# Optimization experiments

Measured on AMD Instinct MI355X. Metric: run time of the kernel, lower is better.

Reference implementation:

```python
import jax, jax.numpy as jnp
import numpy as np

DIM = 128
N = 8192
E = 262144
EPS = 1e-8  # torch.cosine_similarity eps


def setup_inputs() -> dict:
    key = jax.random.key(0)
    k1, k2, k3, k4 = jax.random.split(key, 4)
    x = jax.random.normal(k1, (N, DIM), dtype=jnp.float32)
    edge_index = jax.random.randint(k2, (2, E), 0, N, dtype=jnp.int32)
    # GCNConv parameters: linear weight (glorot-ish) and bias
    W_gcn = jax.random.normal(k3, (DIM, DIM), dtype=jnp.float32) / np.sqrt(DIM)
    b_gcn = jnp.zeros((DIM,), dtype=jnp.float32)
    return {"x": x, "edge_index": edge_index, "W_gcn": W_gcn, "b_gcn": b_gcn}


def _cosine_attention(x):
    # torch.cosine_similarity(x.unsqueeze(1), x.unsqueeze(0), dim=-1)
    # == (x @ x.T) / max(||x_i|| * ||x_j||, eps)
    nrm = jnp.sqrt(jnp.sum(x * x, axis=-1))                      # [N]
    denom = jnp.maximum(nrm[:, None] * nrm[None, :], EPS)        # [N, N]
    sim = (x @ x.T) / denom                                      # [N, N]
    return jax.nn.sigmoid(sim @ x)                               # [N, dim]


def _gcn_conv(x, edge_index, W, b):
    n = x.shape[0]
    xw = x @ W                                                   # [N, dim]
    # add self-loops
    loops = jnp.arange(n, dtype=edge_index.dtype)
    row = jnp.concatenate([edge_index[0], loops])                # source
    col = jnp.concatenate([edge_index[1], loops])                # target
    # symmetric normalization: deg computed on target nodes
    deg = jax.ops.segment_sum(jnp.ones_like(col, dtype=x.dtype), col, num_segments=n)
    dis = jnp.where(deg > 0, jax.lax.rsqrt(jnp.maximum(deg, 1.0)), 0.0)
    dis = jnp.where(deg > 0, deg ** -0.5, 0.0)
    norm = dis[row] * dis[col]                                   # [E+N]
    msgs = xw[row] * norm[:, None]                               # [E+N, dim]
    out = jax.ops.segment_sum(msgs, col, num_segments=n)         # [N, dim]
    return out + b


def reference(x, edge_index, W_gcn, b_gcn):
    att = _cosine_attention(x)
    g = _gcn_conv(x, edge_index, W_gcn, b_gcn)
    return g * att
```

## Files before the change

kernel.cpp:

```cpp
#include <hip/hip_runtime.h>
#include <math.h>

#define NN   8192
#define DIM  128
#define NE   262144
#define XU   64
#define JCH  128
#define HBH  64
#define HEB  (NE / HBH)
#define GU   128
#define GR   64
#define SD   96
#define MSCALE 1048576.0f
#define MINV  (1.0f / 1048576.0f)

typedef __attribute__((ext_vector_type(8))) short bf16x8;
typedef __attribute__((ext_vector_type(4))) float f32x4;

static __device__ __forceinline__ unsigned short f2bf(float f) {
  unsigned int u = __float_as_uint(f);
  return (unsigned short)((u + 0x7FFFu + ((u >> 16) & 1u)) >> 16);
}
static __device__ __forceinline__ float bf2f(unsigned int h) {
  return __uint_as_float(h << 16);
}
static __device__ __forceinline__ unsigned int pk2(float a, float b) {
  return (unsigned int)f2bf(a) | ((unsigned int)f2bf(b) << 16);
}


static __device__ void ph_xtx(int u, int tid, char* smem,
    const float* __restrict__ x, float* __restrict__ rinv,
    int* __restrict__ Mi) {
  char* XTs = smem;
  char* XTu = smem + 32768;
  int j0 = u * JCH;
  int jl = tid >> 1, half = tid & 1;
  const float4* xr = (const float4*)(x + (size_t)(j0 + jl) * DIM + half * 64);
  float ss = 0.f;
  #pragma unroll
  for (int i = 0; i < 16; ++i) {
    float4 v = xr[i];
    ss += v.x * v.x + v.y * v.y + v.z * v.z + v.w * v.w;
  }
  ss += __shfl_xor(ss, 1);
  float rv = 1.0f / sqrtf(ss);
  if (half == 0) rinv[j0 + jl] = rv;
  #pragma unroll
  for (int c4 = 0; c4 < 16; ++c4) {
    float4 v = xr[c4];
    #pragma unroll
    for (int i = 0; i < 4; ++i) {
      int d = half * 64 + c4 * 4 + i;
      float f = ((const float*)&v)[i];
      int off = d * 256 + ((jl * 2) ^ ((d & 7) << 4));
      *(unsigned short*)(XTs + off) = f2bf(f * rv);
      *(unsigned short*)(XTu + off) = f2bf(f);
    }
  }
  __syncthreads();

  int w = tid >> 6, lane = tid & 63;
  int l15 = lane & 15, g16 = (lane >> 4) * 16, swz = (lane & 7) << 4;
  f32x4 acc[2][8];
  #pragma unroll
  for (int dt = 0; dt < 2; ++dt)
    #pragma unroll
    for (int ct = 0; ct < 8; ++ct) acc[dt][ct] = (f32x4){0.f, 0.f, 0.f, 0.f};
  #pragma unroll
  for (int ks = 0; ks < 4; ++ks) {
    int ko = (ks * 64 + g16) ^ swz;
    bf16x8 a0 = *(const bf16x8*)(XTs + (w * 32 + l15) * 256 + ko);
    bf16x8 a1 = *(const bf16x8*)(XTs + (w * 32 + 16 + l15) * 256 + ko);
    #pragma unroll
    for (int ct = 0; ct < 8; ++ct) {
      bf16x8 b = *(const bf16x8*)(XTu + (ct * 16 + l15) * 256 + ko);
      acc[0][ct] = __builtin_amdgcn_mfma_f32_16x16x32_bf16(a0, b, acc[0][ct], 0, 0, 0);
      acc[1][ct] = __builtin_amdgcn_mfma_f32_16x16x32_bf16(a1, b, acc[1][ct], 0, 0, 0);
    }
  }
  #pragma unroll
  for (int dt = 0; dt < 2; ++dt)
    #pragma unroll
    for (int ct = 0; ct < 8; ++ct)
      #pragma unroll
      for (int r = 0; r < 4; ++r) {
        int row = w * 32 + dt * 16 + (lane >> 4) * 4 + r;
        int col = ct * 16 + l15;
        atomicAdd(&Mi[row * DIM + col],
                  __float2int_rn(acc[dt][ct][r] * MSCALE));
      }
}

static __device__ void ph_histplace(int h, int tid, int* ldeg,
    const int* __restrict__ ei, int* __restrict__ gcnt,
    int* __restrict__ sorted) {
  int4* lz = (int4*)ldeg;
  #pragma unroll
  for (int i = tid; i < NN / 4; i += 256) lz[i] = make_int4(0, 0, 0, 0);
  __syncthreads();
  int e0 = h * HEB + tid * 16;
  int4 c0 = *(const int4*)(ei + NE + e0);
  int4 c1 = *(const int4*)(ei + NE + e0 + 4);
  int4 c2 = *(const int4*)(ei + NE + e0 + 8);
  int4 c3 = *(const int4*)(ei + NE + e0 + 12);
  int4 s0 = *(const int4*)(ei + e0);
  int4 s1 = *(const int4*)(ei + e0 + 4);
  int4 s2 = *(const int4*)(ei + e0 + 8);
  int4 s3 = *(const int4*)(ei + e0 + 12);
  int r0  = atomicAdd(&ldeg[c0.x], 1);
  int r1  = atomicAdd(&ldeg[c0.y], 1);
  int r2  = atomicAdd(&ldeg[c0.z], 1);
  int r3  = atomicAdd(&ldeg[c0.w], 1);
  int r4  = atomicAdd(&ldeg[c1.x], 1);
  int r5  = atomicAdd(&ldeg[c1.y], 1);
  int r6  = atomicAdd(&ldeg[c1.z], 1);
  int r7  = atomicAdd(&ldeg[c1.w], 1);
  int r8  = atomicAdd(&ldeg[c2.x], 1);
  int r9  = atomicAdd(&ldeg[c2.y], 1);
  int r10 = atomicAdd(&ldeg[c2.z], 1);
  int r11 = atomicAdd(&ldeg[c2.w], 1);
  int r12 = atomicAdd(&ldeg[c3.x], 1);
  int r13 = atomicAdd(&ldeg[c3.y], 1);
  int r14 = atomicAdd(&ldeg[c3.z], 1);
  int r15 = atomicAdd(&ldeg[c3.w], 1);
  __syncthreads();
  int binb = tid * 32;
  #pragma unroll
  for (int i = 0; i < 8; ++i) {
    int4 v = *(int4*)&ldeg[binb + i * 4];
    if (v.x) ldeg[binb + i * 4 + 0] = atomicAdd(&gcnt[binb + i * 4 + 0], v.x);
    if (v.y) ldeg[binb + i * 4 + 1] = atomicAdd(&gcnt[binb + i * 4 + 1], v.y);
    if (v.z) ldeg[binb + i * 4 + 2] = atomicAdd(&gcnt[binb + i * 4 + 2], v.z);
    if (v.w) ldeg[binb + i * 4 + 3] = atomicAdd(&gcnt[binb + i * 4 + 3], v.w);
  }
  __syncthreads();
  sorted[c0.x * SD + ldeg[c0.x] + r0]  = s0.x;
  sorted[c0.y * SD + ldeg[c0.y] + r1]  = s0.y;
  sorted[c0.z * SD + ldeg[c0.z] + r2]  = s0.z;
  sorted[c0.w * SD + ldeg[c0.w] + r3]  = s0.w;
  sorted[c1.x * SD + ldeg[c1.x] + r4]  = s1.x;
  sorted[c1.y * SD + ldeg[c1.y] + r5]  = s1.y;
  sorted[c1.z * SD + ldeg[c1.z] + r6]  = s1.z;
  sorted[c1.w * SD + ldeg[c1.w] + r7]  = s1.w;
  sorted[c2.x * SD + ldeg[c2.x] + r8]  = s2.x;
  sorted[c2.y * SD + ldeg[c2.y] + r9]  = s2.y;
  sorted[c2.z * SD + ldeg[c2.z] + r10] = s2.z;
  sorted[c2.w * SD + ldeg[c2.w] + r11] = s2.w;
  sorted[c3.x * SD + ldeg[c3.x] + r12] = s3.x;
  sorted[c3.y * SD + ldeg[c3.y] + r13] = s3.y;
  sorted[c3.z * SD + ldeg[c3.z] + r14] = s3.z;
  sorted[c3.w * SD + ldeg[c3.w] + r15] = s3.w;
}

static __device__ void ph_wt(int b, int tid, float* smemf,
    const float* __restrict__ W, unsigned short* __restrict__ Bg) {
  float4* dst = (float4*)smemf;
  const float4* src = (const float4*)(W + (size_t)b * 32 * DIM);
  #pragma unroll
  for (int i = 0; i < 4; ++i) dst[tid + 256 * i] = src[tid + 256 * i];
  __syncthreads();
  int j = tid >> 1, kh = (tid & 1) * 16;
  uint4 p0, p1;
  p0.x = pk2(smemf[(kh + 0) * DIM + j],  smemf[(kh + 1) * DIM + j]);
  p0.y = pk2(smemf[(kh + 2) * DIM + j],  smemf[(kh + 3) * DIM + j]);
  p0.z = pk2(smemf[(kh + 4) * DIM + j],  smemf[(kh + 5) * DIM + j]);
  p0.w = pk2(smemf[(kh + 6) * DIM + j],  smemf[(kh + 7) * DIM + j]);
  p1.x = pk2(smemf[(kh + 8) * DIM + j],  smemf[(kh + 9) * DIM + j]);
  p1.y = pk2(smemf[(kh + 10) * DIM + j], smemf[(kh + 11) * DIM + j]);
  p1.z = pk2(smemf[(kh + 12) * DIM + j], smemf[(kh + 13) * DIM + j]);
  p1.w = pk2(smemf[(kh + 14) * DIM + j], smemf[(kh + 15) * DIM + j]);
  uint4* op = (uint4*)(Bg + (size_t)j * DIM + b * 32 + kh);
  op[0] = p0; op[1] = p1;
}

static __device__ void ph_gemm(int u, int tid, char* smem,
    const float* __restrict__ x, const unsigned short* __restrict__ Bg,
    const int* __restrict__ Mi, const float* __restrict__ rinv,
    const int* __restrict__ gcnt, unsigned short* __restrict__ xws,
    float* __restrict__ att) {
  char* A = smem;
  float* rvs = (float*)(smem + 16384);
  float* dss = rvs + 64;
  int row0 = u * GR;
  #pragma unroll
  for (int i = 0; i < 4; ++i) {
    int c = tid + 256 * i;
    int row = c >> 4, kc = c & 15;
    const float4* s = (const float4*)(x + (size_t)(row0 + row) * DIM + kc * 8);
    float4 v0 = s[0], v1 = s[1];
    uint4 p;
    p.x = pk2(v0.x, v0.y); p.y = pk2(v0.z, v0.w);
    p.z = pk2(v1.x, v1.y); p.w = pk2(v1.z, v1.w);
    *(uint4*)(A + row * 256 + ((kc * 16) ^ ((row & 7) << 4))) = p;
  }
  if (tid < 64) {
    rvs[tid] = rinv[row0 + tid];
    dss[tid] = rsqrtf((float)(gcnt[row0 + tid] + 1));
  }

  int w = tid >> 6, lane = tid & 63;
  int l15 = lane & 15, g16 = (lane >> 4) * 16, swz = (lane & 7) << 4;
  bf16x8 breg[4][4];
  if (w < 2) {
    const char* Bgb = (const char*)Bg;
    #pragma unroll
    for (int ct = 0; ct < 4; ++ct) {
      int j = w * 64 + ct * 16 + l15;
      #pragma unroll
      for (int ks = 0; ks < 4; ++ks)
        breg[ct][ks] = *(const bf16x8*)(Bgb + j * 256 + ks * 64 + g16);
    }
  } else {
    int ge = (lane >> 4) * 8;
    #pragma unroll
    for (int ct = 0; ct < 4; ++ct) {
      int j = (w - 2) * 64 + ct * 16 + l15;
      #pragma unroll
      for (int ks = 0; ks < 4; ++ks) {
        const int4* mp = (const int4*)(Mi + j * DIM + ks * 32 + ge);
        int4 q0 = mp[0], q1 = mp[1];
        union { unsigned int u[4]; bf16x8 v; } uu;
        uu.u[0] = pk2((float)q0.x * MINV, (float)q0.y * MINV);
        uu.u[1] = pk2((float)q0.z * MINV, (float)q0.w * MINV);
        uu.u[2] = pk2((float)q1.x * MINV, (float)q1.y * MINV);
        uu.u[3] = pk2((float)q1.z * MINV, (float)q1.w * MINV);
        breg[ct][ks] = uu.v;
      }
    }
  }
  __syncthreads();

  f32x4 acc[4][4];
  #pragma unroll
  for (int rt = 0; rt < 4; ++rt)
    #pragma unroll
    for (int ct = 0; ct < 4; ++ct) acc[rt][ct] = (f32x4){0.f, 0.f, 0.f, 0.f};
  #pragma unroll
  for (int rt = 0; rt < 4; ++rt) {
    #pragma unroll
    for (int ks = 0; ks < 4; ++ks) {
      bf16x8 a = *(const bf16x8*)(A + (rt * 16 + l15) * 256 + ((ks * 64 + g16) ^ swz));
      #pragma unroll
      for (int ct = 0; ct < 4; ++ct)
        acc[rt][ct] = __builtin_amdgcn_mfma_f32_16x16x32_bf16(a, breg[ct][ks], acc[rt][ct], 0, 0, 0);
    }
  }

  bool isW = (w < 2);
  #pragma unroll
  for (int rt = 0; rt < 4; ++rt)
    #pragma unroll
    for (int ct = 0; ct < 4; ++ct)
      #pragma unroll
      for (int r = 0; r < 4; ++r) {
        int rl = rt * 16 + (lane >> 4) * 4 + r;
        int row = row0 + rl;
        int col = w * 64 + ct * 16 + l15;
        float v = acc[rt][ct][r];
        if (isW) {
          xws[(size_t)row * DIM + col] = f2bf(v * dss[rl]);
        } else {
          float gv = 1.0f / (1.0f + __expf(-v * rvs[rl]));
          att[(size_t)row * DIM + (col - 128)] = gv;
        }
      }
}

__global__ __launch_bounds__(256) void k_pA(const float* __restrict__ x,
    const int* __restrict__ ei, const float* __restrict__ W,
    float* __restrict__ rinv, int* __restrict__ Mi,
    int* __restrict__ gcnt, int* __restrict__ sorted,
    unsigned short* __restrict__ Bg) {
  __shared__ float smem[16512];
  int u = blockIdx.x, tid = threadIdx.x;
  if (u < XU)            ph_xtx(u, tid, (char*)smem, x, rinv, Mi);
  else if (u < XU + HBH) ph_histplace(u - XU, tid, (int*)smem, ei, gcnt, sorted);
  else                   ph_wt(u - XU - HBH, tid, smem, W, Bg);
}
__global__ __launch_bounds__(256) void k_pG(const float* __restrict__ x,
    const unsigned short* __restrict__ Bg, const int* __restrict__ Mi,
    const float* __restrict__ rinv, const int* __restrict__ gcnt,
    unsigned short* __restrict__ xws, float* __restrict__ att) {
  __shared__ float smem[4224];
  ph_gemm(blockIdx.x, threadIdx.x, (char*)smem, x, Bg, Mi, rinv, gcnt, xws, att);
}
__global__ __launch_bounds__(64) void k_pD(const int* __restrict__ gcnt,
    const unsigned short* __restrict__ xws, const float* __restrict__ att,
    const float* __restrict__ bias, const int* __restrict__ sorted,
    float* __restrict__ out) {
  int c = blockIdx.x, t = threadIdx.x;
  int base = c * SD;
  int cnt  = gcnt[c];
  const unsigned int* xw2 = (const unsigned int*)xws;
  unsigned int sv = xw2[(size_t)c * 64 + t];
  float acc0 = bf2f(sv & 0xffffu), acc1 = bf2f(sv >> 16);
  int k = 0;
  for (; k + 8 <= cnt; k += 8) {
    int4 i0 = *(const int4*)(sorted + base + k);
    int4 i1 = *(const int4*)(sorted + base + k + 4);
    unsigned int v0 = xw2[(size_t)i0.x * 64 + t];
    unsigned int v1 = xw2[(size_t)i0.y * 64 + t];
    unsigned int v2 = xw2[(size_t)i0.z * 64 + t];
    unsigned int v3 = xw2[(size_t)i0.w * 64 + t];
    unsigned int v4 = xw2[(size_t)i1.x * 64 + t];
    unsigned int v5 = xw2[(size_t)i1.y * 64 + t];
    unsigned int v6 = xw2[(size_t)i1.z * 64 + t];
    unsigned int v7 = xw2[(size_t)i1.w * 64 + t];
    acc0 += bf2f(v0 & 0xffffu) + bf2f(v1 & 0xffffu) + bf2f(v2 & 0xffffu) + bf2f(v3 & 0xffffu)
          + bf2f(v4 & 0xffffu) + bf2f(v5 & 0xffffu) + bf2f(v6 & 0xffffu) + bf2f(v7 & 0xffffu);
    acc1 += bf2f(v0 >> 16) + bf2f(v1 >> 16) + bf2f(v2 >> 16) + bf2f(v3 >> 16)
          + bf2f(v4 >> 16) + bf2f(v5 >> 16) + bf2f(v6 >> 16) + bf2f(v7 >> 16);
  }
  for (; k + 4 <= cnt; k += 4) {
    int4 i0 = *(const int4*)(sorted + base + k);
    unsigned int v0 = xw2[(size_t)i0.x * 64 + t];
    unsigned int v1 = xw2[(size_t)i0.y * 64 + t];
    unsigned int v2 = xw2[(size_t)i0.z * 64 + t];
    unsigned int v3 = xw2[(size_t)i0.w * 64 + t];
    acc0 += bf2f(v0 & 0xffffu) + bf2f(v1 & 0xffffu) + bf2f(v2 & 0xffffu) + bf2f(v3 & 0xffffu);
    acc1 += bf2f(v0 >> 16) + bf2f(v1 >> 16) + bf2f(v2 >> 16) + bf2f(v3 >> 16);
  }
  for (; k < cnt; ++k) {
    unsigned int v = xw2[(size_t)sorted[base + k] * 64 + t];
    acc0 += bf2f(v & 0xffffu);
    acc1 += bf2f(v >> 16);
  }
  float dc = rsqrtf((float)(cnt + 1));
  float2 at = ((const float2*)att)[(size_t)c * 64 + t];
  float2 bs = ((const float2*)bias)[t];
  float2 o;
  o.x = (acc0 * dc + bs.x) * at.x;
  o.y = (acc1 * dc + bs.y) * at.y;
  ((float2*)out)[(size_t)c * 64 + t] = o;
}

extern "C" void kernel_launch(void* const* d_in, const int* in_sizes, int n_in,
                              void* d_out, int out_size, void* d_ws, size_t ws_size,
                              hipStream_t stream) {
  const float* x  = (const float*)d_in[0];
  const int*   ei = (const int*)  d_in[1];
  const float* W  = (const float*)d_in[2];
  const float* b  = (const float*)d_in[3];
  float* out = (float*)d_out;

  unsigned short* xws = (unsigned short*)d_ws;
  float* att   = (float*)(xws + (size_t)NN * DIM);
  unsigned short* Bg = (unsigned short*)(att + (size_t)NN * DIM);
  int*   Mi    = (int*)(Bg + DIM * DIM);
  int*   gcnt  = Mi + DIM * DIM;
  float* rinv  = (float*)(gcnt + NN);
  int*   sorted= (int*)(rinv + NN);

  (void)hipMemsetAsync(Mi, 0, (DIM * DIM + NN) * sizeof(int), stream);

  k_pA<<<XU + HBH + 4, 256, 0, stream>>>(x, ei, W, rinv, Mi, gcnt, sorted, Bg);
  k_pG<<<GU, 256, 0, stream>>>(x, Bg, Mi, rinv, gcnt, xws, att);
  k_pD<<<NN, 64, 0, stream>>>(gcnt, xws, att, b, sorted, out);
}
```

Before: 106.2 us.

## Move edge histogram/placement into GEMM kernel, apply source-degree scaling in gather

```diff
diff --git a/kernel.cpp b/kernel.cpp
--- a/kernel.cpp
+++ b/kernel.cpp
@@ -177,11 +177,9 @@
 static __device__ void ph_gemm(int u, int tid, char* smem,
     const float* __restrict__ x, const unsigned short* __restrict__ Bg,
     const int* __restrict__ Mi, const float* __restrict__ rinv,
-    const int* __restrict__ gcnt, unsigned short* __restrict__ xws,
-    float* __restrict__ att) {
+    unsigned short* __restrict__ xws, float* __restrict__ att) {
   char* A = smem;
   float* rvs = (float*)(smem + 16384);
-  float* dss = rvs + 64;
   int row0 = u * GR;
   #pragma unroll
   for (int i = 0; i < 4; ++i) {
@@ -194,10 +192,7 @@
     p.z = pk2(v1.x, v1.y); p.w = pk2(v1.z, v1.w);
     *(uint4*)(A + row * 256 + ((kc * 16) ^ ((row & 7) << 4))) = p;
   }
-  if (tid < 64) {
-    rvs[tid] = rinv[row0 + tid];
-    dss[tid] = rsqrtf((float)(gcnt[row0 + tid] + 1));
-  }
+  if (tid < 64) rvs[tid] = rinv[row0 + tid];
 
   int w = tid >> 6, lane = tid & 63;
   int l15 = lane & 15, g16 = (lane >> 4) * 16, swz = (lane & 7) << 4;
@@ -259,7 +254,7 @@
         int col = w * 64 + ct * 16 + l15;
         float v = acc[rt][ct][r];
         if (isW) {
-          xws[(size_t)row * DIM + col] = f2bf(v * dss[rl]);
+          xws[(size_t)row * DIM + col] = f2bf(v);
         } else {
           float gv = 1.0f / (1.0f + __expf(-v * rvs[rl]));
           att[(size_t)row * DIM + (col - 128)] = gv;
@@ -268,22 +263,22 @@
 }
 
 __global__ __launch_bounds__(256) void k_pA(const float* __restrict__ x,
-    const int* __restrict__ ei, const float* __restrict__ W,
-    float* __restrict__ rinv, int* __restrict__ Mi,
-    int* __restrict__ gcnt, int* __restrict__ sorted,
-    unsigned short* __restrict__ Bg) {
+    const float* __restrict__ W, float* __restrict__ rinv,
+    int* __restrict__ Mi, unsigned short* __restrict__ Bg) {
   __shared__ float smem[16512];
   int u = blockIdx.x, tid = threadIdx.x;
-  if (u < XU)            ph_xtx(u, tid, (char*)smem, x, rinv, Mi);
-  else if (u < XU + HBH) ph_histplace(u - XU, tid, (int*)smem, ei, gcnt, sorted);
-  else                   ph_wt(u - XU - HBH, tid, smem, W, Bg);
+  if (u < XU) ph_xtx(u, tid, (char*)smem, x, rinv, Mi);
+  else        ph_wt(u - XU, tid, smem, W, Bg);
 }
 __global__ __launch_bounds__(256) void k_pG(const float* __restrict__ x,
-    const unsigned short* __restrict__ Bg, const int* __restrict__ Mi,
-    const float* __restrict__ rinv, const int* __restrict__ gcnt,
+    const int* __restrict__ ei, const unsigned short* __restrict__ Bg,
+    const int* __restrict__ Mi, const float* __restrict__ rinv,
+    int* __restrict__ gcnt, int* __restrict__ sorted,
     unsigned short* __restrict__ xws, float* __restrict__ att) {
-  __shared__ float smem[4224];
-  ph_gemm(blockIdx.x, threadIdx.x, (char*)smem, x, Bg, Mi, rinv, gcnt, xws, att);
+  __shared__ float smem[8192];
+  int u = blockIdx.x, tid = threadIdx.x;
+  if (u < GU) ph_gemm(u, tid, (char*)smem, x, Bg, Mi, rinv, xws, att);
+  else        ph_histplace(u - GU, tid, (int*)smem, ei, gcnt, sorted);
 }
 __global__ __launch_bounds__(64) void k_pD(const int* __restrict__ gcnt,
     const unsigned short* __restrict__ xws, const float* __restrict__ att,
@@ -292,13 +287,22 @@
   int c = blockIdx.x, t = threadIdx.x;
   int base = c * SD;
   int cnt  = gcnt[c];
+  float dcs = rsqrtf((float)(cnt + 1));
   const unsigned int* xw2 = (const unsigned int*)xws;
   unsigned int sv = xw2[(size_t)c * 64 + t];
-  float acc0 = bf2f(sv & 0xffffu), acc1 = bf2f(sv >> 16);
+  float acc0 = bf2f(sv & 0xffffu) * dcs, acc1 = bf2f(sv >> 16) * dcs;
   int k = 0;
   for (; k + 8 <= cnt; k += 8) {
     int4 i0 = *(const int4*)(sorted + base + k);
     int4 i1 = *(const int4*)(sorted + base + k + 4);
+    float d0 = rsqrtf((float)(gcnt[i0.x] + 1));
+    float d1 = rsqrtf((float)(gcnt[i0.y] + 1));
+    float d2 = rsqrtf((float)(gcnt[i0.z] + 1));
+    float d3 = rsqrtf((float)(gcnt[i0.w] + 1));
+    float d4 = rsqrtf((float)(gcnt[i1.x] + 1));
+    float d5 = rsqrtf((float)(gcnt[i1.y] + 1));
+    float d6 = rsqrtf((float)(gcnt[i1.z] + 1));
+    float d7 = rsqrtf((float)(gcnt[i1.w] + 1));
     unsigned int v0 = xw2[(size_t)i0.x * 64 + t];
     unsigned int v1 = xw2[(size_t)i0.y * 64 + t];
     unsigned int v2 = xw2[(size_t)i0.z * 64 + t];
@@ -307,31 +311,42 @@
     unsigned int v5 = xw2[(size_t)i1.y * 64 + t];
     unsigned int v6 = xw2[(size_t)i1.z * 64 + t];
     unsigned int v7 = xw2[(size_t)i1.w * 64 + t];
-    acc0 += bf2f(v0 & 0xffffu) + bf2f(v1 & 0xffffu) + bf2f(v2 & 0xffffu) + bf2f(v3 & 0xffffu)
-          + bf2f(v4 & 0xffffu) + bf2f(v5 & 0xffffu) + bf2f(v6 & 0xffffu) + bf2f(v7 & 0xffffu);
-    acc1 += bf2f(v0 >> 16) + bf2f(v1 >> 16) + bf2f(v2 >> 16) + bf2f(v3 >> 16)
-          + bf2f(v4 >> 16) + bf2f(v5 >> 16) + bf2f(v6 >> 16) + bf2f(v7 >> 16);
+    acc0 += bf2f(v0 & 0xffffu) * d0 + bf2f(v1 & 0xffffu) * d1
+          + bf2f(v2 & 0xffffu) * d2 + bf2f(v3 & 0xffffu) * d3
+          + bf2f(v4 & 0xffffu) * d4 + bf2f(v5 & 0xffffu) * d5
+          + bf2f(v6 & 0xffffu) * d6 + bf2f(v7 & 0xffffu) * d7;
+    acc1 += bf2f(v0 >> 16) * d0 + bf2f(v1 >> 16) * d1
+          + bf2f(v2 >> 16) * d2 + bf2f(v3 >> 16) * d3
+          + bf2f(v4 >> 16) * d4 + bf2f(v5 >> 16) * d5
+          + bf2f(v6 >> 16) * d6 + bf2f(v7 >> 16) * d7;
   }
   for (; k + 4 <= cnt; k += 4) {
     int4 i0 = *(const int4*)(sorted + base + k);
+    float d0 = rsqrtf((float)(gcnt[i0.x] + 1));
+    float d1 = rsqrtf((float)(gcnt[i0.y] + 1));
+    float d2 = rsqrtf((float)(gcnt[i0.z] + 1));
+    float d3 = rsqrtf((float)(gcnt[i0.w] + 1));
     unsigned int v0 = xw2[(size_t)i0.x * 64 + t];
     unsigned int v1 = xw2[(size_t)i0.y * 64 + t];
     unsigned int v2 = xw2[(size_t)i0.z * 64 + t];
     unsigned int v3 = xw2[(size_t)i0.w * 64 + t];
-    acc0 += bf2f(v0 & 0xffffu) + bf2f(v1 & 0xffffu) + bf2f(v2 & 0xffffu) + bf2f(v3 & 0xffffu);
-    acc1 += bf2f(v0 >> 16) + bf2f(v1 >> 16) + bf2f(v2 >> 16) + bf2f(v3 >> 16);
+    acc0 += bf2f(v0 & 0xffffu) * d0 + bf2f(v1 & 0xffffu) * d1
+          + bf2f(v2 & 0xffffu) * d2 + bf2f(v3 & 0xffffu) * d3;
+    acc1 += bf2f(v0 >> 16) * d0 + bf2f(v1 >> 16) * d1
+          + bf2f(v2 >> 16) * d2 + bf2f(v3 >> 16) * d3;
   }
   for (; k < cnt; ++k) {
-    unsigned int v = xw2[(size_t)sorted[base + k] * 64 + t];
-    acc0 += bf2f(v & 0xffffu);
-    acc1 += bf2f(v >> 16);
-  }
-  float dc = rsqrtf((float)(cnt + 1));
+    int s = sorted[base + k];
+    float dn = rsqrtf((float)(gcnt[s] + 1));
+    unsigned int v = xw2[(size_t)s * 64 + t];
+    acc0 += bf2f(v & 0xffffu) * dn;
+    acc1 += bf2f(v >> 16) * dn;
+  }
   float2 at = ((const float2*)att)[(size_t)c * 64 + t];
   float2 bs = ((const float2*)bias)[t];
   float2 o;
-  o.x = (acc0 * dc + bs.x) * at.x;
-  o.y = (acc1 * dc + bs.y) * at.y;
+  o.x = (acc0 * dcs + bs.x) * at.x;
+  o.y = (acc1 * dcs + bs.y) * at.y;
   ((float2*)out)[(size_t)c * 64 + t] = o;
 }
 
@@ -354,7 +369,7 @@
 
   (void)hipMemsetAsync(Mi, 0, (DIM * DIM + NN) * sizeof(int), stream);
 
-  k_pA<<<XU + HBH + 4, 256, 0, stream>>>(x, ei, W, rinv, Mi, gcnt, sorted, Bg);
-  k_pG<<<GU, 256, 0, stream>>>(x, Bg, Mi, rinv, gcnt, xws, att);
+  k_pA<<<XU + 4, 256, 0, stream>>>(x, W, rinv, Mi, Bg);
+  k_pG<<<GU + HBH, 256, 0, stream>>>(x, ei, Bg, Mi, rinv, gcnt, sorted, xws, att);
   k_pD<<<NN, 64, 0, stream>>>(gcnt, xws, att, b, sorted, out);
 }
```

After: 106.1 us. No clear change (-0.1%).
